# Performance work log

Measured on AMD Instinct MI355X. Metric: run time of the kernel, lower is better.

Reference implementation:

```python
import jax, jax.numpy as jnp
import numpy as np

N_NODES = 100000
H_DIM = 128
N_RELS = 90   # num_rels*2 inside RGCN
N_BASES = 4
N_EDGES = 800000


def setup_inputs() -> dict:
    key = jax.random.key(0)
    k_emb, k_w, k_comp, k_r, k_norm, k_src, k_dst, k_b = jax.random.split(key, 8)
    h = jnp.arange(N_NODES, dtype=jnp.int64 if jax.config.jax_enable_x64 else jnp.int32)
    r = jax.random.randint(k_r, (N_EDGES,), 0, N_RELS)
    norm = jax.random.uniform(k_norm, (N_EDGES, 1), dtype=jnp.float32)
    src = jax.random.randint(k_src, (N_EDGES,), 0, N_NODES)
    dst = jax.random.randint(k_dst, (N_EDGES,), 0, N_NODES)
    # learned params (embedding table stands in for the word2vec-initialized table)
    emb_table = jax.random.normal(k_emb, (N_NODES, H_DIM), dtype=jnp.float32) * 0.02
    weight = jax.random.normal(k_w, (N_BASES, H_DIM, H_DIM), dtype=jnp.float32) * (1.0 / np.sqrt(H_DIM))
    w_comp = jax.random.normal(k_comp, (N_RELS, N_BASES), dtype=jnp.float32) * 0.5
    h_bias = jnp.zeros((H_DIM,), dtype=jnp.float32)
    return {"h": h, "r": r, "norm": norm, "src": src, "dst": dst,
            "emb_table": emb_table, "weight": weight, "w_comp": w_comp, "h_bias": h_bias}


def reference(h, r, norm, src, dst, emb_table, weight, w_comp, h_bias):
    # Input layer: embedding lookup on node ids  -> [N, D]
    x = emb_table[h]
    # Basis decomposition: project node feats onto each basis once  -> [N, B, D]
    # (avoids materializing per-edge [D,D] relation matrices)
    xb = jnp.einsum('ni,bio->nbo', x, weight)
    # Per-edge message: combine basis projections with relation coefficients
    coeff = w_comp[r]                       # [E, B]
    msg = jnp.einsum('ebo,eb->eo', xb[src], coeff)   # [E, D]
    msg = msg * norm                        # edge norm [E,1]
    # scatter-mean over destination nodes
    agg = jax.ops.segment_sum(msg, dst, num_segments=N_NODES)          # [N, D]
    cnt = jax.ops.segment_sum(jnp.ones((msg.shape[0],), msg.dtype), dst,
                              num_segments=N_NODES)                    # [N]
    node_repr = agg / jnp.maximum(cnt, 1.0)[:, None]
    # bias (RelGraphConv default bias=True); activation=None, self_loop=False, dropout=0
    node_repr = node_repr + h_bias
    return node_repr
```

## Files before the change

kernel.cpp:

```cpp
#include <hip/hip_runtime.h>
#include <hip/hip_bf16.h>

#define N_NODES 100000
#define H_DIM   128
#define N_RELS  90
#define N_BASES 4
#define N_EDGES 800000
#define SCAN_NB 391
#define NBLK    6250

typedef __attribute__((ext_vector_type(8))) __bf16 bf16x8;
typedef __attribute__((ext_vector_type(4))) float  floatx4;

#define WT_OFF     0
#define CNTS_OFF   131072
#define OFFS_OFF   531072
#define CURS_OFF   931072
#define BSUM_OFF   1331072
#define FLAG_OFF   1332672
#define RECS_OFF   1334272

__device__ __forceinline__ float bs2f(unsigned short s) {
    union { unsigned u; float f; } x; x.u = ((unsigned)s) << 16; return x.f;
}
__device__ __forceinline__ unsigned short f2bs(float f) {
    unsigned u = __float_as_uint(f);
    return (unsigned short)((u + 0x7fffu + ((u >> 16) & 1u)) >> 16);
}
__device__ __forceinline__ float ldf(const void* p, size_t i, int isbf) {
    return isbf ? bs2f(((const unsigned short*)p)[i]) : ((const float*)p)[i];
}
__device__ __forceinline__ int detect_bf(const void* norm) {
    const unsigned* w = (const unsigned*)norm;
    int hits = 0;
#pragma unroll
    for (int i = 0; i < 16; ++i) {
        unsigned b1 = (w[i] >> 8) & 0xffu;
        hits += (b1 >= 0x30u && b1 <= 0x3fu) ? 1 : 0;
    }
    return hits >= 12;
}

__global__ __launch_bounds__(256) void prep_count_k(const void* __restrict__ weight,
                                                    unsigned short* __restrict__ wt,
                                                    const int* __restrict__ dst,
                                                    int* __restrict__ counts,
                                                    const void* __restrict__ norm,
                                                    int* __restrict__ flag) {
    int b = blockIdx.x;
    if (b == 0 && threadIdx.x == 0) *flag = detect_bf(norm);
    if (b < 256) {
        int isbf = detect_bf(norm);
        int tid = b * 256 + threadIdx.x;
        int o = tid >> 9, c = tid & 511;
        int bb = c >> 7, i = c & 127;
        wt[tid] = f2bs(ldf(weight, (size_t)bb * 16384 + (size_t)i * 128 + o, isbf));
    } else {
        int e = (b - 256) * 256 + threadIdx.x;
        if (e < N_EDGES) atomicAdd(&counts[dst[e]], 1);
    }
}

__global__ __launch_bounds__(256) void scanA(const int* __restrict__ counts,
                                             int* __restrict__ offs, int* __restrict__ bsum) {
    __shared__ int s[256];
    int t = threadIdx.x, i = blockIdx.x * 256 + t;
    int v = (i < N_NODES) ? counts[i] : 0;
    s[t] = v; __syncthreads();
    for (int off = 1; off < 256; off <<= 1) {
        int x = (t >= off) ? s[t - off] : 0;
        __syncthreads(); s[t] += x; __syncthreads();
    }
    if (i < N_NODES) offs[i] = s[t] - v;
    if (t == 255) bsum[blockIdx.x] = s[255];
}

__global__ __launch_bounds__(256) void scanC2(int* __restrict__ offs,
                                              const int* __restrict__ bsum,
                                              int* __restrict__ cursor) {
    int b = blockIdx.x, t = threadIdx.x;
    int v = 0;
    if (t < b) v = bsum[t];
    if (t + 256 < b) v += bsum[t + 256];
    v += __shfl_down(v, 32); v += __shfl_down(v, 16);
    v += __shfl_down(v, 8);  v += __shfl_down(v, 4);
    v += __shfl_down(v, 2);  v += __shfl_down(v, 1);
    __shared__ int wsum[4];
    __shared__ int sprefix;
    if ((t & 63) == 0) wsum[t >> 6] = v;
    __syncthreads();
    if (t == 0) sprefix = wsum[0] + wsum[1] + wsum[2] + wsum[3];
    __syncthreads();
    int i = b * 256 + t;
    if (i < N_NODES) {
        int o = offs[i] + sprefix;
        offs[i] = o; cursor[i] = o;
    }
}

__global__ __launch_bounds__(256) void fill_k(const int* __restrict__ r, const void* __restrict__ norm,
                                              const int* __restrict__ src, const int* __restrict__ dst,
                                              const int* __restrict__ h,
                                              int* __restrict__ cursor,
                                              unsigned long long* __restrict__ recs) {
    int e = blockIdx.x * 256 + threadIdx.x;
    if (e >= N_EDGES) return;
    int isbf = detect_bf(norm);
    float nm = ldf(norm, e, isbf);
    unsigned lo = (unsigned)h[src[e]] | ((unsigned)r[e] << 20);
    unsigned long long rc = (unsigned long long)lo
                          | ((unsigned long long)__float_as_uint(nm) << 32);
    int pos = atomicAdd(&cursor[dst[e]], 1);
    __builtin_nontemporal_store(rc, &recs[pos]);
}

template <int ISBF>
__global__ __launch_bounds__(256) void fused_k(const int* __restrict__ counts,
                                               const int* __restrict__ offs,
                                               const unsigned long long* __restrict__ recs,
                                               const void* __restrict__ emb,
                                               const unsigned short* __restrict__ wt,
                                               const void* __restrict__ bias,
                                               const void* __restrict__ wcomp,
                                               const int* __restrict__ flag,
                                               void* __restrict__ out) {
    if ((*flag != 0) != (ISBF != 0)) return;
    __shared__ float wc[N_RELS * 4];
    __shared__ __align__(16) unsigned short y[16][520];
    for (int t = threadIdx.x; t < N_RELS * 4; t += 256) wc[t] = ldf(wcomp, t, ISBF);
    __syncthreads();

    int t = threadIdx.x;
    int lane = t & 63;
    int w = t >> 6;
    int g = lane >> 4, j = lane & 15;
    int blk = blockIdx.x;
    int dloc = w * 4 + g;
    int d = blk * 16 + dloc;
    int deg = counts[d], start = offs[d];
    float inv = 1.0f / (float)(deg > 1 ? deg : 1);

    float acc[4][8];
#pragma unroll
    for (int b = 0; b < 4; ++b)
#pragma unroll
        for (int c = 0; c < 8; ++c) acc[b][c] = 0.f;

    int kmax = __shfl(deg, 0);
    kmax = max(kmax, __shfl(deg, 16));
    kmax = max(kmax, __shfl(deg, 32));
    kmax = max(kmax, __shfl(deg, 48));

    unsigned long long rcur[4];
#pragma unroll
    for (int u = 0; u < 4; ++u)
        rcur[u] = __builtin_nontemporal_load(&recs[(u < deg) ? start + u : 0]);

    for (int k = 0; k < kmax; k += 4) {
        unsigned long long rnext[4];
#pragma unroll
        for (int u = 0; u < 4; ++u) {
            int kk = k + 4 + u;
            rnext[u] = __builtin_nontemporal_load(&recs[(kk < deg) ? start + kk : 0]);
        }
        bf16x8  rb[4];
        floatx4 rf[4][2];
        if (ISBF) {
#pragma unroll
            for (int u = 0; u < 4; ++u) {
                unsigned hx = (unsigned)rcur[u] & 0xFFFFFu;
                rb[u] = *(const bf16x8*)((const unsigned short*)emb + (size_t)hx * 128 + j * 8);
            }
        } else {
#pragma unroll
            for (int u = 0; u < 4; ++u) {
                unsigned hx = (unsigned)rcur[u] & 0xFFFFFu;
                const floatx4* f = (const floatx4*)((const float*)emb + (size_t)hx * 128 + j * 8);
                rf[u][0] = f[0]; rf[u][1] = f[1];
            }
        }
#pragma unroll
        for (int u = 0; u < 4; ++u) {
            bool v = (k + u) < deg;
            unsigned rel = ((unsigned)rcur[u] >> 20) & 0xFFFu;
            float nm = v ? __uint_as_float((unsigned)(rcur[u] >> 32)) : 0.f;
            const float* cw = &wc[rel * 4];
            float c0 = cw[0] * nm, c1 = cw[1] * nm, c2 = cw[2] * nm, c3 = cw[3] * nm;
            float x[8];
            if (ISBF) {
#pragma unroll
                for (int c = 0; c < 8; ++c) x[c] = (float)rb[u][c];
            } else {
#pragma unroll
                for (int c = 0; c < 4; ++c) { x[c] = rf[u][0][c]; x[c + 4] = rf[u][1][c]; }
            }
#pragma unroll
            for (int c = 0; c < 8; ++c) {
                acc[0][c] += c0 * x[c];
                acc[1][c] += c1 * x[c];
                acc[2][c] += c2 * x[c];
                acc[3][c] += c3 * x[c];
            }
        }
#pragma unroll
        for (int u = 0; u < 4; ++u) rcur[u] = rnext[u];
    }

#pragma unroll
    for (int b = 0; b < 4; ++b) {
        union { unsigned short u[8]; uint4 v; } pk;
#pragma unroll
        for (int c = 0; c < 8; ++c) pk.u[c] = f2bs(acc[b][c] * inv);
        *(uint4*)&y[dloc][b * 128 + j * 8] = pk.v;
    }
    __syncthreads();

    int m = lane & 15;
    int q = lane >> 4;
    for (int half = 0; half < 2; ++half) {
        int ct = w * 2 + half;
        floatx4 accm = {0.f, 0.f, 0.f, 0.f};
        const unsigned short* bp = wt + (size_t)(ct * 16 + m) * 512 + q * 8;
#pragma unroll
        for (int kc = 0; kc < 16; ++kc) {
            bf16x8 af = *(const bf16x8*)&y[m][kc * 32 + q * 8];
            bf16x8 bf = *(const bf16x8*)(bp + kc * 32);
            accm = __builtin_amdgcn_mfma_f32_16x16x32_bf16(af, bf, accm, 0, 0, 0);
        }
#pragma unroll
        for (int v = 0; v < 4; ++v) {
            int o = ct * 16 + m;
            float val = accm[v] + ldf(bias, o, ISBF);
            size_t oi = (size_t)(blk * 16 + q * 4 + v) * H_DIM + o;
            if (ISBF) __builtin_nontemporal_store(f2bs(val), (unsigned short*)out + oi);
            else      __builtin_nontemporal_store(val, (float*)out + oi);
        }
    }
}

extern "C" void kernel_launch(void* const* d_in, const int* in_sizes, int n_in,
                              void* d_out, int out_size, void* d_ws, size_t ws_size,
                              hipStream_t stream) {
    const int*  h      = (const int*)d_in[0];
    const int*  r      = (const int*)d_in[1];
    const void* norm   = d_in[2];
    const int*  src    = (const int*)d_in[3];
    const int*  dst    = (const int*)d_in[4];
    const void* emb    = d_in[5];
    const void* weight = d_in[6];
    const void* wcomp  = d_in[7];
    const void* bias   = d_in[8];

    char* ws = (char*)d_ws;
    unsigned short*     wt     = (unsigned short*)(ws + WT_OFF);
    int*                counts = (int*)(ws + CNTS_OFF);
    int*                offs   = (int*)(ws + OFFS_OFF);
    int*                cursor = (int*)(ws + CURS_OFF);
    int*                bsum   = (int*)(ws + BSUM_OFF);
    int*                flag   = (int*)(ws + FLAG_OFF);
    unsigned long long* recs   = (unsigned long long*)(ws + RECS_OFF);

    hipMemsetAsync(counts, 0, N_NODES * sizeof(int), stream);

    prep_count_k<<<256 + (N_EDGES + 255) / 256, 256, 0, stream>>>(weight, wt, dst, counts,
                                                                  norm, flag);
    scanA<<<SCAN_NB, 256, 0, stream>>>(counts, offs, bsum);
    scanC2<<<SCAN_NB, 256, 0, stream>>>(offs, bsum, cursor);
    fill_k<<<(N_EDGES + 255) / 256, 256, 0, stream>>>(r, norm, src, dst, h, cursor, recs);
    fused_k<1><<<NBLK, 256, 0, stream>>>(counts, offs, recs, emb, wt, bias, wcomp, flag, d_out);
    fused_k<0><<<NBLK, 256, 0, stream>>>(counts, offs, recs, emb, wt, bias, wcomp, flag, d_out);
}
```

Before: 338.8 us.

## Host-side dtype dispatch, identity-id shortcut, and double-buffered gather pipeline

The bf16/fp32 choice now comes from the host using the input byte size, so only one fused kernel is launched and the device-side dtype sniffing goes away. A device flag checks whether h is the identity; when it is, fill_k uses src directly and skips the h[src] gather. The fused aggregation loop now double-buffers the embedding-row loads so the next batch of rows is in flight while the current one is accumulated. Nontemporal loads and stores were also swapped for plain ones. The cost is higher register pressure from the two row buffers.

```diff
diff --git a/kernel.cpp b/kernel.cpp
--- a/kernel.cpp
+++ b/kernel.cpp
@@ -14,11 +14,11 @@
 
 #define WT_OFF     0
 #define CNTS_OFF   131072
-#define OFFS_OFF   531072
-#define CURS_OFF   931072
-#define BSUM_OFF   1331072
-#define FLAG_OFF   1332672
-#define RECS_OFF   1334272
+#define IDF_OFF    531072
+#define OFFS_OFF   531076
+#define CURS_OFF   931076
+#define BSUM_OFF   1331076
+#define RECS_OFF   1332640
 
 __device__ __forceinline__ float bs2f(unsigned short s) {
     union { unsigned u; float f; } x; x.u = ((unsigned)s) << 16; return x.f;
@@ -27,37 +27,29 @@
     unsigned u = __float_as_uint(f);
     return (unsigned short)((u + 0x7fffu + ((u >> 16) & 1u)) >> 16);
 }
-__device__ __forceinline__ float ldf(const void* p, size_t i, int isbf) {
-    return isbf ? bs2f(((const unsigned short*)p)[i]) : ((const float*)p)[i];
-}
-__device__ __forceinline__ int detect_bf(const void* norm) {
-    const unsigned* w = (const unsigned*)norm;
-    int hits = 0;
-#pragma unroll
-    for (int i = 0; i < 16; ++i) {
-        unsigned b1 = (w[i] >> 8) & 0xffu;
-        hits += (b1 >= 0x30u && b1 <= 0x3fu) ? 1 : 0;
-    }
-    return hits >= 12;
-}
-
+template <int ISBF>
+__device__ __forceinline__ float ldT(const void* p, size_t i) {
+    if (ISBF) return bs2f(((const unsigned short*)p)[i]);
+    return ((const float*)p)[i];
+}
+
+template <int ISBF>
 __global__ __launch_bounds__(256) void prep_count_k(const void* __restrict__ weight,
                                                     unsigned short* __restrict__ wt,
                                                     const int* __restrict__ dst,
                                                     int* __restrict__ counts,
-                                                    const void* __restrict__ norm,
-                                                    int* __restrict__ flag) {
+                                                    const int* __restrict__ h,
+                                                    int* __restrict__ idflag) {
     int b = blockIdx.x;
-    if (b == 0 && threadIdx.x == 0) *flag = detect_bf(norm);
     if (b < 256) {
-        int isbf = detect_bf(norm);
         int tid = b * 256 + threadIdx.x;
         int o = tid >> 9, c = tid & 511;
         int bb = c >> 7, i = c & 127;
-        wt[tid] = f2bs(ldf(weight, (size_t)bb * 16384 + (size_t)i * 128 + o, isbf));
+        wt[tid] = f2bs(ldT<ISBF>(weight, (size_t)bb * 16384 + (size_t)i * 128 + o));
     } else {
         int e = (b - 256) * 256 + threadIdx.x;
         if (e < N_EDGES) atomicAdd(&counts[dst[e]], 1);
+        if (e < N_NODES && h[e] != e) atomicOr(idflag, 1);
     }
 }
 
@@ -98,20 +90,22 @@
     }
 }
 
+template <int ISBF>
 __global__ __launch_bounds__(256) void fill_k(const int* __restrict__ r, const void* __restrict__ norm,
                                               const int* __restrict__ src, const int* __restrict__ dst,
-                                              const int* __restrict__ h,
+                                              const int* __restrict__ h, const int* __restrict__ idflag,
                                               int* __restrict__ cursor,
                                               unsigned long long* __restrict__ recs) {
     int e = blockIdx.x * 256 + threadIdx.x;
     if (e >= N_EDGES) return;
-    int isbf = detect_bf(norm);
-    float nm = ldf(norm, e, isbf);
-    unsigned lo = (unsigned)h[src[e]] | ((unsigned)r[e] << 20);
+    float nm = ldT<ISBF>(norm, e);
+    int s = src[e];
+    int hs = (*idflag) ? h[s] : s;
+    unsigned lo = (unsigned)hs | ((unsigned)r[e] << 20);
     unsigned long long rc = (unsigned long long)lo
                           | ((unsigned long long)__float_as_uint(nm) << 32);
     int pos = atomicAdd(&cursor[dst[e]], 1);
-    __builtin_nontemporal_store(rc, &recs[pos]);
+    recs[pos] = rc;
 }
 
 template <int ISBF>
@@ -122,12 +116,10 @@
                                                const unsigned short* __restrict__ wt,
                                                const void* __restrict__ bias,
                                                const void* __restrict__ wcomp,
-                                               const int* __restrict__ flag,
                                                void* __restrict__ out) {
-    if ((*flag != 0) != (ISBF != 0)) return;
     __shared__ float wc[N_RELS * 4];
     __shared__ __align__(16) unsigned short y[16][520];
-    for (int t = threadIdx.x; t < N_RELS * 4; t += 256) wc[t] = ldf(wcomp, t, ISBF);
+    for (int t = threadIdx.x; t < N_RELS * 4; t += 256) wc[t] = ldT<ISBF>(wcomp, t);
     __syncthreads();
 
     int t = threadIdx.x;
@@ -151,60 +143,80 @@
     kmax = max(kmax, __shfl(deg, 32));
     kmax = max(kmax, __shfl(deg, 48));
 
-    unsigned long long rcur[4];
-#pragma unroll
-    for (int u = 0; u < 4; ++u)
-        rcur[u] = __builtin_nontemporal_load(&recs[(u < deg) ? start + u : 0]);
-
-    for (int k = 0; k < kmax; k += 4) {
-        unsigned long long rnext[4];
-#pragma unroll
-        for (int u = 0; u < 4; ++u) {
-            int kk = k + 4 + u;
-            rnext[u] = __builtin_nontemporal_load(&recs[(kk < deg) ? start + kk : 0]);
-        }
-        bf16x8  rb[4];
-        floatx4 rf[4][2];
-        if (ISBF) {
-#pragma unroll
-            for (int u = 0; u < 4; ++u) {
-                unsigned hx = (unsigned)rcur[u] & 0xFFFFFu;
-                rb[u] = *(const bf16x8*)((const unsigned short*)emb + (size_t)hx * 128 + j * 8);
-            }
-        } else {
-#pragma unroll
-            for (int u = 0; u < 4; ++u) {
-                unsigned hx = (unsigned)rcur[u] & 0xFFFFFu;
-                const floatx4* f = (const floatx4*)((const float*)emb + (size_t)hx * 128 + j * 8);
-                rf[u][0] = f[0]; rf[u][1] = f[1];
-            }
-        }
-#pragma unroll
-        for (int u = 0; u < 4; ++u) {
-            bool v = (k + u) < deg;
-            unsigned rel = ((unsigned)rcur[u] >> 20) & 0xFFFu;
-            float nm = v ? __uint_as_float((unsigned)(rcur[u] >> 32)) : 0.f;
-            const float* cw = &wc[rel * 4];
-            float c0 = cw[0] * nm, c1 = cw[1] * nm, c2 = cw[2] * nm, c3 = cw[3] * nm;
-            float x[8];
-            if (ISBF) {
-#pragma unroll
-                for (int c = 0; c < 8; ++c) x[c] = (float)rb[u][c];
-            } else {
-#pragma unroll
-                for (int c = 0; c < 4; ++c) { x[c] = rf[u][0][c]; x[c + 4] = rf[u][1][c]; }
-            }
-#pragma unroll
-            for (int c = 0; c < 8; ++c) {
-                acc[0][c] += c0 * x[c];
-                acc[1][c] += c1 * x[c];
-                acc[2][c] += c2 * x[c];
-                acc[3][c] += c3 * x[c];
-            }
-        }
-#pragma unroll
-        for (int u = 0; u < 4; ++u) rcur[u] = rnext[u];
-    }
+    unsigned long long rcur[4], rnext[4], rfut[4];
+    bf16x8  rbA[4], rbB[4];
+    floatx4 rfA[4][2], rfB[4][2];
+
+#define LOADRECS(DST, KB)                                                     \
+    do {                                                                      \
+        _Pragma("unroll") for (int u = 0; u < 4; ++u) {                       \
+            int kk = (KB) + u;                                                \
+            DST[u] = recs[(kk < deg) ? start + kk : 0];                       \
+        }                                                                     \
+    } while (0)
+
+#define LOADROWS(RB, RF, RV)                                                  \
+    do {                                                                      \
+        if (ISBF) {                                                           \
+            _Pragma("unroll") for (int u = 0; u < 4; ++u) {                   \
+                unsigned hx = (unsigned)RV[u] & 0xFFFFFu;                     \
+                RB[u] = *(const bf16x8*)((const unsigned short*)emb           \
+                                         + (size_t)hx * 128 + j * 8);         \
+            }                                                                 \
+        } else {                                                              \
+            _Pragma("unroll") for (int u = 0; u < 4; ++u) {                   \
+                unsigned hx = (unsigned)RV[u] & 0xFFFFFu;                     \
+                const floatx4* f = (const floatx4*)((const float*)emb         \
+                                         + (size_t)hx * 128 + j * 8);         \
+                RF[u][0] = f[0]; RF[u][1] = f[1];                             \
+            }                                                                 \
+        }                                                                     \
+    } while (0)
+
+#define CONSUME(RB, RF, RV, KB)                                               \
+    do {                                                                      \
+        _Pragma("unroll") for (int u = 0; u < 4; ++u) {                       \
+            bool vld = ((KB) + u) < deg;                                      \
+            unsigned rel = ((unsigned)RV[u] >> 20) & 0xFFFu;                  \
+            float nm = vld ? __uint_as_float((unsigned)(RV[u] >> 32)) : 0.f;  \
+            const float* cw = &wc[rel * 4];                                   \
+            float c0 = cw[0]*nm, c1 = cw[1]*nm, c2 = cw[2]*nm, c3 = cw[3]*nm; \
+            float x[8];                                                       \
+            if (ISBF) {                                                       \
+                _Pragma("unroll") for (int c = 0; c < 8; ++c)                 \
+                    x[c] = (float)RB[u][c];                                   \
+            } else {                                                          \
+                _Pragma("unroll") for (int c = 0; c < 4; ++c) {               \
+                    x[c] = RF[u][0][c]; x[c + 4] = RF[u][1][c];               \
+                }                                                             \
+            }                                                                 \
+            _Pragma("unroll") for (int c = 0; c < 8; ++c) {                   \
+                acc[0][c] += c0 * x[c]; acc[1][c] += c1 * x[c];               \
+                acc[2][c] += c2 * x[c]; acc[3][c] += c3 * x[c];               \
+            }                                                                 \
+        }                                                                     \
+    } while (0)
+
+    LOADRECS(rcur, 0);
+    LOADROWS(rbA, rfA, rcur);
+    LOADRECS(rnext, 4);
+
+    for (int k = 0; k < kmax; k += 8) {
+        LOADROWS(rbB, rfB, rnext);
+        LOADRECS(rfut, k + 8);
+        CONSUME(rbA, rfA, rcur, k);
+#pragma unroll
+        for (int u = 0; u < 4; ++u) { rcur[u] = rnext[u]; rnext[u] = rfut[u]; }
+        if (k + 4 >= kmax) break;
+        LOADROWS(rbA, rfA, rnext);
+        LOADRECS(rfut, k + 12);
+        CONSUME(rbB, rfB, rcur, k + 4);
+#pragma unroll
+        for (int u = 0; u < 4; ++u) { rcur[u] = rnext[u]; rnext[u] = rfut[u]; }
+    }
+#undef LOADRECS
+#undef LOADROWS
+#undef CONSUME
 
 #pragma unroll
     for (int b = 0; b < 4; ++b) {
@@ -230,12 +242,36 @@
 #pragma unroll
         for (int v = 0; v < 4; ++v) {
             int o = ct * 16 + m;
-            float val = accm[v] + ldf(bias, o, ISBF);
+            float val = accm[v] + ldT<ISBF>(bias, o);
             size_t oi = (size_t)(blk * 16 + q * 4 + v) * H_DIM + o;
-            if (ISBF) __builtin_nontemporal_store(f2bs(val), (unsigned short*)out + oi);
-            else      __builtin_nontemporal_store(val, (float*)out + oi);
+            if (ISBF) ((unsigned short*)out)[oi] = f2bs(val);
+            else      ((float*)out)[oi] = val;
         }
     }
+}
+
+template <int ISBF>
+static void launch_all(const int* h, const int* r, const void* norm, const int* src,
+                       const int* dst, const void* emb, const void* weight,
+                       const void* wcomp, const void* bias, char* ws, void* d_out,
+                       hipStream_t stream) {
+    unsigned short*     wt     = (unsigned short*)(ws + WT_OFF);
+    int*                counts = (int*)(ws + CNTS_OFF);
+    int*                idflag = (int*)(ws + IDF_OFF);
+    int*                offs   = (int*)(ws + OFFS_OFF);
+    int*                cursor = (int*)(ws + CURS_OFF);
+    int*                bsum   = (int*)(ws + BSUM_OFF);
+    unsigned long long* recs   = (unsigned long long*)(ws + RECS_OFF);
+
+    hipMemsetAsync(counts, 0, N_NODES * sizeof(int) + sizeof(int), stream);
+
+    prep_count_k<ISBF><<<256 + (N_EDGES + 255) / 256, 256, 0, stream>>>(weight, wt, dst,
+                                                                        counts, h, idflag);
+    scanA<<<SCAN_NB, 256, 0, stream>>>(counts, offs, bsum);
+    scanC2<<<SCAN_NB, 256, 0, stream>>>(offs, bsum, cursor);
+    fill_k<ISBF><<<(N_EDGES + 255) / 256, 256, 0, stream>>>(r, norm, src, dst, h, idflag,
+                                                            cursor, recs);
+    fused_k<ISBF><<<NBLK, 256, 0, stream>>>(counts, offs, recs, emb, wt, bias, wcomp, d_out);
 }
 
 extern "C" void kernel_launch(void* const* d_in, const int* in_sizes, int n_in,
@@ -250,23 +286,10 @@
     const void* weight = d_in[6];
     const void* wcomp  = d_in[7];
     const void* bias   = d_in[8];
-
     char* ws = (char*)d_ws;
-    unsigned short*     wt     = (unsigned short*)(ws + WT_OFF);
-    int*                counts = (int*)(ws + CNTS_OFF);
-    int*                offs   = (int*)(ws + OFFS_OFF);
-    int*                cursor = (int*)(ws + CURS_OFF);
-    int*                bsum   = (int*)(ws + BSUM_OFF);
-    int*                flag   = (int*)(ws + FLAG_OFF);
-    unsigned long long* recs   = (unsigned long long*)(ws + RECS_OFF);
-
-    hipMemsetAsync(counts, 0, N_NODES * sizeof(int), stream);
-
-    prep_count_k<<<256 + (N_EDGES + 255) / 256, 256, 0, stream>>>(weight, wt, dst, counts,
-                                                                  norm, flag);
-    scanA<<<SCAN_NB, 256, 0, stream>>>(counts, offs, bsum);
-    scanC2<<<SCAN_NB, 256, 0, stream>>>(offs, bsum, cursor);
-    fill_k<<<(N_EDGES + 255) / 256, 256, 0, stream>>>(r, norm, src, dst, h, cursor, recs);
-    fused_k<1><<<NBLK, 256, 0, stream>>>(counts, offs, recs, emb, wt, bias, wcomp, flag, d_out);
-    fused_k<0><<<NBLK, 256, 0, stream>>>(counts, offs, recs, emb, wt, bias, wcomp, flag, d_out);
-}
+
+    int isbf = (in_sizes[2] == (int)(N_EDGES * sizeof(unsigned short))) ? 1 : 0;
+
+    if (isbf) launch_all<1>(h, r, norm, src, dst, emb, weight, wcomp, bias, ws, d_out, stream);
+    else      launch_all<0>(h, r, norm, src, dst, emb, weight, wcomp, bias, ws, d_out, stream);
+}
```

Result: no change. 342.3 us (+1.1%).

## Choose dtype on host, prefetch embedding rows one step ahead, skip identity h gather

Applied to the files above, without the earlier changes.

Picks bf16 or fp32 on the host from the input byte size, so only one fused kernel is launched instead of two with a device flag check, and the per-thread dtype detection goes away. The gather loop now software-pipelines the embedding row loads one group of four edges ahead, and record loads two groups ahead, to hide gather latency at the cost of more registers. An identity check on h lets fill_k skip the h[src] indirection when h is arange, which adds an atomicOr in the count kernel. Output stores switch from nontemporal to normal stores.

```diff
diff --git a/kernel.cpp b/kernel.cpp
--- a/kernel.cpp
+++ b/kernel.cpp
@@ -14,11 +14,11 @@
 
 #define WT_OFF     0
 #define CNTS_OFF   131072
-#define OFFS_OFF   531072
-#define CURS_OFF   931072
-#define BSUM_OFF   1331072
-#define FLAG_OFF   1332672
-#define RECS_OFF   1334272
+#define IDF_OFF    531072
+#define OFFS_OFF   531076
+#define CURS_OFF   931076
+#define BSUM_OFF   1331076
+#define RECS_OFF   1332640
 
 __device__ __forceinline__ float bs2f(unsigned short s) {
     union { unsigned u; float f; } x; x.u = ((unsigned)s) << 16; return x.f;
@@ -27,37 +27,29 @@
     unsigned u = __float_as_uint(f);
     return (unsigned short)((u + 0x7fffu + ((u >> 16) & 1u)) >> 16);
 }
-__device__ __forceinline__ float ldf(const void* p, size_t i, int isbf) {
-    return isbf ? bs2f(((const unsigned short*)p)[i]) : ((const float*)p)[i];
-}
-__device__ __forceinline__ int detect_bf(const void* norm) {
-    const unsigned* w = (const unsigned*)norm;
-    int hits = 0;
-#pragma unroll
-    for (int i = 0; i < 16; ++i) {
-        unsigned b1 = (w[i] >> 8) & 0xffu;
-        hits += (b1 >= 0x30u && b1 <= 0x3fu) ? 1 : 0;
-    }
-    return hits >= 12;
-}
-
+template <int ISBF>
+__device__ __forceinline__ float ldT(const void* p, size_t i) {
+    if (ISBF) return bs2f(((const unsigned short*)p)[i]);
+    return ((const float*)p)[i];
+}
+
+template <int ISBF>
 __global__ __launch_bounds__(256) void prep_count_k(const void* __restrict__ weight,
                                                     unsigned short* __restrict__ wt,
                                                     const int* __restrict__ dst,
                                                     int* __restrict__ counts,
-                                                    const void* __restrict__ norm,
-                                                    int* __restrict__ flag) {
+                                                    const int* __restrict__ h,
+                                                    int* __restrict__ idflag) {
     int b = blockIdx.x;
-    if (b == 0 && threadIdx.x == 0) *flag = detect_bf(norm);
     if (b < 256) {
-        int isbf = detect_bf(norm);
         int tid = b * 256 + threadIdx.x;
         int o = tid >> 9, c = tid & 511;
         int bb = c >> 7, i = c & 127;
-        wt[tid] = f2bs(ldf(weight, (size_t)bb * 16384 + (size_t)i * 128 + o, isbf));
+        wt[tid] = f2bs(ldT<ISBF>(weight, (size_t)bb * 16384 + (size_t)i * 128 + o));
     } else {
         int e = (b - 256) * 256 + threadIdx.x;
         if (e < N_EDGES) atomicAdd(&counts[dst[e]], 1);
+        if (e < N_NODES && h[e] != e) atomicOr(idflag, 1);
     }
 }
 
@@ -98,16 +90,18 @@
     }
 }
 
+template <int ISBF>
 __global__ __launch_bounds__(256) void fill_k(const int* __restrict__ r, const void* __restrict__ norm,
                                               const int* __restrict__ src, const int* __restrict__ dst,
-                                              const int* __restrict__ h,
+                                              const int* __restrict__ h, const int* __restrict__ idflag,
                                               int* __restrict__ cursor,
                                               unsigned long long* __restrict__ recs) {
     int e = blockIdx.x * 256 + threadIdx.x;
     if (e >= N_EDGES) return;
-    int isbf = detect_bf(norm);
-    float nm = ldf(norm, e, isbf);
-    unsigned lo = (unsigned)h[src[e]] | ((unsigned)r[e] << 20);
+    float nm = ldT<ISBF>(norm, e);
+    int s = src[e];
+    int hs = (*idflag) ? h[s] : s;
+    unsigned lo = (unsigned)hs | ((unsigned)r[e] << 20);
     unsigned long long rc = (unsigned long long)lo
                           | ((unsigned long long)__float_as_uint(nm) << 32);
     int pos = atomicAdd(&cursor[dst[e]], 1);
@@ -122,12 +116,10 @@
                                                const unsigned short* __restrict__ wt,
                                                const void* __restrict__ bias,
                                                const void* __restrict__ wcomp,
-                                               const int* __restrict__ flag,
                                                void* __restrict__ out) {
-    if ((*flag != 0) != (ISBF != 0)) return;
     __shared__ float wc[N_RELS * 4];
     __shared__ __align__(16) unsigned short y[16][520];
-    for (int t = threadIdx.x; t < N_RELS * 4; t += 256) wc[t] = ldf(wcomp, t, ISBF);
+    for (int t = threadIdx.x; t < N_RELS * 4; t += 256) wc[t] = ldT<ISBF>(wcomp, t);
     __syncthreads();
 
     int t = threadIdx.x;
@@ -151,49 +143,62 @@
     kmax = max(kmax, __shfl(deg, 32));
     kmax = max(kmax, __shfl(deg, 48));
 
-    unsigned long long rcur[4];
+    unsigned long long rcur[4], rnext[4];
+    bf16x8  rows[4];
+    floatx4 rowsf[4][2];
+
 #pragma unroll
     for (int u = 0; u < 4; ++u)
         rcur[u] = __builtin_nontemporal_load(&recs[(u < deg) ? start + u : 0]);
+    if (ISBF) {
+#pragma unroll
+        for (int u = 0; u < 4; ++u) {
+            unsigned hx = (unsigned)rcur[u] & 0xFFFFFu;
+            rows[u] = *(const bf16x8*)((const unsigned short*)emb + (size_t)hx * 128 + j * 8);
+        }
+    } else {
+#pragma unroll
+        for (int u = 0; u < 4; ++u) {
+            unsigned hx = (unsigned)rcur[u] & 0xFFFFFu;
+            const floatx4* f = (const floatx4*)((const float*)emb + (size_t)hx * 128 + j * 8);
+            rowsf[u][0] = f[0]; rowsf[u][1] = f[1];
+        }
+    }
+#pragma unroll
+    for (int u = 0; u < 4; ++u) {
+        int kk = 4 + u;
+        rnext[u] = __builtin_nontemporal_load(&recs[(kk < deg) ? start + kk : 0]);
+    }
 
     for (int k = 0; k < kmax; k += 4) {
-        unsigned long long rnext[4];
-#pragma unroll
-        for (int u = 0; u < 4; ++u) {
-            int kk = k + 4 + u;
-            rnext[u] = __builtin_nontemporal_load(&recs[(kk < deg) ? start + kk : 0]);
-        }
-        bf16x8  rb[4];
-        floatx4 rf[4][2];
-        if (ISBF) {
-#pragma unroll
-            for (int u = 0; u < 4; ++u) {
-                unsigned hx = (unsigned)rcur[u] & 0xFFFFFu;
-                rb[u] = *(const bf16x8*)((const unsigned short*)emb + (size_t)hx * 128 + j * 8);
+#pragma unroll
+        for (int u = 0; u < 4; ++u) {
+            float x[8];
+            if (ISBF) {
+                bf16x8 rv = rows[u];
+#pragma unroll
+                for (int c = 0; c < 8; ++c) x[c] = (float)rv[c];
+            } else {
+                floatx4 a = rowsf[u][0], bvec = rowsf[u][1];
+#pragma unroll
+                for (int c = 0; c < 4; ++c) { x[c] = a[c]; x[c + 4] = bvec[c]; }
             }
-        } else {
-#pragma unroll
-            for (int u = 0; u < 4; ++u) {
-                unsigned hx = (unsigned)rcur[u] & 0xFFFFFu;
-                const floatx4* f = (const floatx4*)((const float*)emb + (size_t)hx * 128 + j * 8);
-                rf[u][0] = f[0]; rf[u][1] = f[1];
+            {
+                unsigned hx = (unsigned)rnext[u] & 0xFFFFFu;
+                if (ISBF) {
+                    rows[u] = *(const bf16x8*)((const unsigned short*)emb
+                                               + (size_t)hx * 128 + j * 8);
+                } else {
+                    const floatx4* f = (const floatx4*)((const float*)emb
+                                               + (size_t)hx * 128 + j * 8);
+                    rowsf[u][0] = f[0]; rowsf[u][1] = f[1];
+                }
             }
-        }
-#pragma unroll
-        for (int u = 0; u < 4; ++u) {
-            bool v = (k + u) < deg;
+            bool vld = (k + u) < deg;
             unsigned rel = ((unsigned)rcur[u] >> 20) & 0xFFFu;
-            float nm = v ? __uint_as_float((unsigned)(rcur[u] >> 32)) : 0.f;
+            float nm = vld ? __uint_as_float((unsigned)(rcur[u] >> 32)) : 0.f;
             const float* cw = &wc[rel * 4];
             float c0 = cw[0] * nm, c1 = cw[1] * nm, c2 = cw[2] * nm, c3 = cw[3] * nm;
-            float x[8];
-            if (ISBF) {
-#pragma unroll
-                for (int c = 0; c < 8; ++c) x[c] = (float)rb[u][c];
-            } else {
-#pragma unroll
-                for (int c = 0; c < 4; ++c) { x[c] = rf[u][0][c]; x[c + 4] = rf[u][1][c]; }
-            }
 #pragma unroll
             for (int c = 0; c < 8; ++c) {
                 acc[0][c] += c0 * x[c];
@@ -204,6 +209,11 @@
         }
 #pragma unroll
         for (int u = 0; u < 4; ++u) rcur[u] = rnext[u];
+#pragma unroll
+        for (int u = 0; u < 4; ++u) {
+            int kk = k + 8 + u;
+            rnext[u] = __builtin_nontemporal_load(&recs[(kk < deg) ? start + kk : 0]);
+        }
     }
 
 #pragma unroll
@@ -230,12 +240,36 @@
 #pragma unroll
         for (int v = 0; v < 4; ++v) {
             int o = ct * 16 + m;
-            float val = accm[v] + ldf(bias, o, ISBF);
+            float val = accm[v] + ldT<ISBF>(bias, o);
             size_t oi = (size_t)(blk * 16 + q * 4 + v) * H_DIM + o;
-            if (ISBF) __builtin_nontemporal_store(f2bs(val), (unsigned short*)out + oi);
-            else      __builtin_nontemporal_store(val, (float*)out + oi);
-        }
-    }
+            if (ISBF) ((unsigned short*)out)[oi] = f2bs(val);
+            else      ((float*)out)[oi] = val;
+        }
+    }
+}
+
+template <int ISBF>
+static void launch_all(const int* h, const int* r, const void* norm, const int* src,
+                       const int* dst, const void* emb, const void* weight,
+                       const void* wcomp, const void* bias, char* ws, void* d_out,
+                       hipStream_t stream) {
+    unsigned short*     wt     = (unsigned short*)(ws + WT_OFF);
+    int*                counts = (int*)(ws + CNTS_OFF);
+    int*                idflag = (int*)(ws + IDF_OFF);
+    int*                offs   = (int*)(ws + OFFS_OFF);
+    int*                cursor = (int*)(ws + CURS_OFF);
+    int*                bsum   = (int*)(ws + BSUM_OFF);
+    unsigned long long* recs   = (unsigned long long*)(ws + RECS_OFF);
+
+    hipMemsetAsync(counts, 0, N_NODES * sizeof(int) + sizeof(int), stream);
+
+    prep_count_k<ISBF><<<256 + (N_EDGES + 255) / 256, 256, 0, stream>>>(weight, wt, dst,
+                                                                        counts, h, idflag);
+    scanA<<<SCAN_NB, 256, 0, stream>>>(counts, offs, bsum);
+    scanC2<<<SCAN_NB, 256, 0, stream>>>(offs, bsum, cursor);
+    fill_k<ISBF><<<(N_EDGES + 255) / 256, 256, 0, stream>>>(r, norm, src, dst, h, idflag,
+                                                            cursor, recs);
+    fused_k<ISBF><<<NBLK, 256, 0, stream>>>(counts, offs, recs, emb, wt, bias, wcomp, d_out);
 }
 
 extern "C" void kernel_launch(void* const* d_in, const int* in_sizes, int n_in,
@@ -250,23 +284,10 @@
     const void* weight = d_in[6];
     const void* wcomp  = d_in[7];
     const void* bias   = d_in[8];
-
     char* ws = (char*)d_ws;
-    unsigned short*     wt     = (unsigned short*)(ws + WT_OFF);
-    int*                counts = (int*)(ws + CNTS_OFF);
-    int*                offs   = (int*)(ws + OFFS_OFF);
-    int*                cursor = (int*)(ws + CURS_OFF);
-    int*                bsum   = (int*)(ws + BSUM_OFF);
-    int*                flag   = (int*)(ws + FLAG_OFF);
-    unsigned long long* recs   = (unsigned long long*)(ws + RECS_OFF);
-
-    hipMemsetAsync(counts, 0, N_NODES * sizeof(int), stream);
-
-    prep_count_k<<<256 + (N_EDGES + 255) / 256, 256, 0, stream>>>(weight, wt, dst, counts,
-                                                                  norm, flag);
-    scanA<<<SCAN_NB, 256, 0, stream>>>(counts, offs, bsum);
-    scanC2<<<SCAN_NB, 256, 0, stream>>>(offs, bsum, cursor);
-    fill_k<<<(N_EDGES + 255) / 256, 256, 0, stream>>>(r, norm, src, dst, h, cursor, recs);
-    fused_k<1><<<NBLK, 256, 0, stream>>>(counts, offs, recs, emb, wt, bias, wcomp, flag, d_out);
-    fused_k<0><<<NBLK, 256, 0, stream>>>(counts, offs, recs, emb, wt, bias, wcomp, flag, d_out);
-}
+
+    int isbf = (in_sizes[2] == (int)(N_EDGES * sizeof(unsigned short))) ? 1 : 0;
+
+    if (isbf) launch_all<1>(h, r, norm, src, dst, emb, weight, wcomp, bias, ws, d_out, stream);
+    else      launch_all<0>(h, r, norm, src, dst, emb, weight, wcomp, bias, ws, d_out, stream);
+}
```

After: 353.1 us. +4.2%, slower.
